# Kernel tuning notes

Hardware: AMD Instinct MI355X
Metric: run time of the kernel (lower is better)

The kernel has to match this reference:

```python
import jax, jax.numpy as jnp
import numpy as np

D_IN = 1024
D_OUT = 1024
NUM_HEADS = 16
HEAD_DIM = D_OUT // NUM_HEADS


def setup_inputs() -> dict:
    key = jax.random.key(0)
    ks = jax.random.split(key, 6)
    scale = 0.02
    x = jax.random.normal(ks[0], (2, 2048, D_IN), dtype=jnp.float32)
    Wq = jax.random.normal(ks[1], (D_IN, D_OUT), dtype=jnp.float32) * scale
    Wk = jax.random.normal(ks[2], (D_IN, D_OUT), dtype=jnp.float32) * scale
    Wv = jax.random.normal(ks[3], (D_IN, D_OUT), dtype=jnp.float32) * scale
    Wo = jax.random.normal(ks[4], (D_OUT, D_OUT), dtype=jnp.float32) * scale
    bo = jax.random.normal(ks[5], (D_OUT,), dtype=jnp.float32) * scale
    return {"x": x, "Wq": Wq, "Wk": Wk, "Wv": Wv, "Wo": Wo, "bo": bo}


def reference(x, Wq, Wk, Wv, Wo, bo):
    b, T, _ = x.shape
    h, dh = NUM_HEADS, HEAD_DIM
    # QKV projections (no bias), split heads: [b,T,d_out] -> [b,h,T,dh]
    q = (x @ Wq).reshape(b, T, h, dh).transpose(0, 2, 1, 3)
    k = (x @ Wk).reshape(b, T, h, dh).transpose(0, 2, 1, 3)
    v = (x @ Wv).reshape(b, T, h, dh).transpose(0, 2, 1, 3)
    # scaled dot-product scores with causal mask
    scores = jnp.einsum("bhqd,bhkd->bhqk", q, k) / jnp.sqrt(jnp.float32(dh))
    causal = jnp.tril(jnp.ones((T, T), dtype=bool))  # True = allowed
    scores = jnp.where(causal, scores, -jnp.inf)
    attn = jax.nn.softmax(scores, axis=-1)
    # dropout p=0.0 -> identity
    ctx = jnp.einsum("bhqk,bhkd->bhqd", attn, v)
    ctx = ctx.transpose(0, 2, 1, 3).reshape(b, T, h * dh)
    return ctx @ Wo + bo
```

## Files before the change

kernel.cpp:

```cpp
#include <hip/hip_runtime.h>

typedef __attribute__((ext_vector_type(8))) __bf16 bf16x8;
typedef __attribute__((ext_vector_type(4))) __bf16 bf16x4;
typedef __attribute__((ext_vector_type(4))) float  f32x4;

static constexpr int TSEQ    = 2048;
static constexpr int DMODEL  = 1024;
static constexpr int HD      = 64;
static constexpr int VSTRIDE = 2080;
static constexpr int LSTR    = 72;

#define AS1 __attribute__((address_space(1)))
#define AS3 __attribute__((address_space(3)))

__global__ __launch_bounds__(256) void k_prep(const float* __restrict__ x,
    const float* __restrict__ w0, const float* __restrict__ w1,
    const float* __restrict__ w2, const float* __restrict__ w3,
    __bf16* __restrict__ xbf, __bf16* __restrict__ wt_all) {
  __shared__ float tile[32][33];
  const int blk = blockIdx.x;
  const int tid = threadIdx.x;
  if (blk < 4096) {
    size_t i = ((size_t)blk * 256 + tid) * 4;
    float4 v = *(const float4*)(x + i);
    bf16x4 o = { (__bf16)v.x, (__bf16)v.y, (__bf16)v.z, (__bf16)v.w };
    *(bf16x4*)(xbf + i) = o;
    return;
  }
  const int tz = blk - 4096;
  const int wi = tz >> 10;
  const int tl = tz & 1023;
  const int n0 = (tl & 31) * 32, k0 = (tl >> 5) * 32;
  const float* w = wi == 0 ? w0 : wi == 1 ? w1 : wi == 2 ? w2 : w3;
  __bf16* out = wt_all + (size_t)wi * DMODEL * DMODEL;
  const int tx = tid & 31, ty0 = (tid >> 5) * 4;
#pragma unroll
  for (int j = 0; j < 4; j++)
    tile[ty0 + j][tx] = w[(size_t)(k0 + ty0 + j) * DMODEL + n0 + tx];
  __syncthreads();
#pragma unroll
  for (int j = 0; j < 4; j++)
    out[(size_t)(n0 + ty0 + j) * DMODEL + k0 + tx] = (__bf16)tile[tx][ty0 + j];
}

template <int NB>
__device__ __forceinline__ void gemm_mainloop_p(const __bf16* __restrict__ A,
                                                const __bf16* __restrict__ Bt,
                                                int bm, int bn,
                                                __bf16* At, __bf16* Bl,
                                                f32x4 acc[4][NB / 32]) {
  constexpr int NT = NB / 32;
  const int tid  = threadIdx.x;
  const int lane = tid & 63;
  const int l15  = lane & 15, quad = lane >> 4;
  const int wv   = tid >> 6;
  const int wm   = (wv >> 1) * 64, wn = (wv & 1) * (NT * 16);
  const int srow = lane >> 2;
  const int scol = (lane & 3) << 3;

  auto stage = [&](int k0, int hb) {
#pragma unroll
    for (int ss = 0; ss < 2; ss++) {
      const int s   = wv * 2 + ss;
      const int row = s * 16 + srow;
      __builtin_amdgcn_global_load_lds(
          (const AS1 void*)(A + (size_t)(bm + row) * 1024 + k0 + scol),
          (AS3 void*)(At + hb * 4096 + s * 512), 16, 0, 0);
    }
#pragma unroll
    for (int ss = 0; ss < NB / 64; ss++) {
      const int s   = wv * (NB / 64) + ss;
      const int row = s * 16 + srow;
      __builtin_amdgcn_global_load_lds(
          (const AS1 void*)(Bt + (size_t)(bn + row) * 1024 + k0 + scol),
          (AS3 void*)(Bl + hb * (NB * 32) + s * 512), 16, 0, 0);
    }
  };

  stage(0, 0);
  for (int k0 = 0; k0 < 1024; k0 += 32) {
    const int cur = (k0 >> 5) & 1;
    __syncthreads();
    bf16x8 af[4], bfr[NT];
#pragma unroll
    for (int mt = 0; mt < 4; mt++)
      af[mt] = *(const bf16x8*)(At + cur * 4096 + (wm + mt * 16 + l15) * 32 + quad * 8);
#pragma unroll
    for (int nt = 0; nt < NT; nt++)
      bfr[nt] = *(const bf16x8*)(Bl + cur * (NB * 32) + (wn + nt * 16 + l15) * 32 + quad * 8);
    if (k0 + 32 < 1024) stage(k0 + 32, cur ^ 1);
#pragma unroll
    for (int mt = 0; mt < 4; mt++)
#pragma unroll
      for (int nt = 0; nt < NT; nt++)
        acc[mt][nt] = __builtin_amdgcn_mfma_f32_16x16x32_bf16(
            af[mt], bfr[nt], acc[mt][nt], 0, 0, 0);
  }
}

__global__ __launch_bounds__(256) void k_gemm_qkv(const __bf16* __restrict__ xbf,
    const __bf16* __restrict__ wt_all, __bf16* __restrict__ qws,
    __bf16* __restrict__ kws, __bf16* __restrict__ vtws) {
  __shared__ __bf16 At[2 * 128 * 32];
  __shared__ __bf16 Bl[2 * 128 * 32];
  const int which = blockIdx.z;
  const __bf16* wt = wt_all + (size_t)which * DMODEL * DMODEL;
  const int bm = blockIdx.y * 128, bn = blockIdx.x * 128;
  f32x4 acc[4][4];
  const f32x4 z = {0.f, 0.f, 0.f, 0.f};
#pragma unroll
  for (int mt = 0; mt < 4; mt++)
#pragma unroll
    for (int nt = 0; nt < 4; nt++) acc[mt][nt] = z;
  gemm_mainloop_p<128>(xbf, wt, bm, bn, At, Bl, acc);
  const int lane = threadIdx.x & 63;
  const int l15 = lane & 15, quad = lane >> 4;
  const int wv = threadIdx.x >> 6;
  const int wm = (wv >> 1) * 64, wn = (wv & 1) * 64;
#pragma unroll
  for (int mt = 0; mt < 4; mt++)
#pragma unroll
    for (int nt = 0; nt < 4; nt++)
#pragma unroll
      for (int r = 0; r < 4; r++) {
        int m = bm + wm + mt * 16 + quad * 4 + r;
        int n = bn + wn + nt * 16 + l15;
        int b = m >> 11, t = m & 2047;
        int h = n >> 6,  d = n & 63;
        int bh = b * 16 + h;
        float av = acc[mt][nt][r];
        if (which == 0)      qws[((size_t)bh * TSEQ + t) * HD + d] = (__bf16)(av * 0.18033688f);
        else if (which == 1) kws[((size_t)bh * TSEQ + t) * HD + d] = (__bf16)av;
        else                 vtws[((size_t)bh * HD + d) * VSTRIDE + t] = (__bf16)av;
      }
}

__global__ __launch_bounds__(256) void k_attn(const __bf16* __restrict__ qws,
    const __bf16* __restrict__ kws, const __bf16* __restrict__ vtws,
    __bf16* __restrict__ ctx) {
  const int bh  = blockIdx.x & 31;
  const int qb0 = blockIdx.x >> 5, qb1 = 31 - qb0;
  const int tid = threadIdx.x;
  const int lane = tid & 63, wv = tid >> 6;
  const int l15 = lane & 15, quad = lane >> 4;
  const __bf16* qp = qws  + (size_t)bh * TSEQ * HD;
  const __bf16* kp = kws  + (size_t)bh * TSEQ * HD;
  const __bf16* vp = vtws + (size_t)bh * HD * VSTRIDE;
  const int b = bh >> 4, h = bh & 15;

  __shared__ __bf16 kbuf[2][64 * LSTR];
  __shared__ __bf16 vbuf[2][64 * LSTR];
  __shared__ __bf16 plds[4][16 * LSTR];

  const f32x4 z = {0.f, 0.f, 0.f, 0.f};
  const int sr = tid >> 3, sc = (tid & 7) * 8;

  const int qr0a = qb0 * 64 + wv * 16;
  const int qr0b = qb1 * 64 + wv * 16;
  bf16x8 aq0[2], aq1[2];
#pragma unroll
  for (int kb = 0; kb < 2; kb++) {
    aq0[kb] = *(const bf16x8*)(qp + (size_t)(qr0a + l15) * HD + kb * 32 + quad * 8);
    aq1[kb] = *(const bf16x8*)(qp + (size_t)(qr0b + l15) * HD + kb * 32 + quad * 8);
  }

  bf16x8 kreg[2], vreg[2];
  kreg[0] = *(const bf16x8*)(kp + (size_t)sr * HD + sc);
  kreg[1] = *(const bf16x8*)(kp + (size_t)(sr + 32) * HD + sc);
  vreg[0] = *(const bf16x8*)(vp + (size_t)sr * VSTRIDE + sc);
  vreg[1] = *(const bf16x8*)(vp + (size_t)(sr + 32) * VSTRIDE + sc);
  *(bf16x8*)(kbuf[0] + sr * LSTR + sc)        = kreg[0];
  *(bf16x8*)(kbuf[0] + (sr + 32) * LSTR + sc) = kreg[1];
  *(bf16x8*)(vbuf[0] + sr * LSTR + sc)        = vreg[0];
  *(bf16x8*)(vbuf[0] + (sr + 32) * LSTR + sc) = vreg[1];
  __syncthreads();

  float lpart[4] = {0.f, 0.f, 0.f, 0.f};
  f32x4 acc[4];
#pragma unroll
  for (int dt = 0; dt < 4; dt++) acc[dt] = z;

  for (int s = 0; s < 33; s++) {
    const int cur = s & 1;
    const bool h0 = (s <= qb0);
    const bool masked = (s == qb0) || (s == 32);

    if (s + 1 < 33) {
      const int ktn = (s + 1 <= qb0) ? (s + 1) * 64 : (s - qb0) * 64;
      kreg[0] = *(const bf16x8*)(kp + (size_t)(ktn + sr) * HD + sc);
      kreg[1] = *(const bf16x8*)(kp + (size_t)(ktn + sr + 32) * HD + sc);
      vreg[0] = *(const bf16x8*)(vp + (size_t)sr * VSTRIDE + ktn + sc);
      vreg[1] = *(const bf16x8*)(vp + (size_t)(sr + 32) * VSTRIDE + ktn + sc);
    }

    const __bf16* kb_ = kbuf[cur];
    const __bf16* vb_ = vbuf[cur];
    f32x4 sarr[4];
#pragma unroll
    for (int nt = 0; nt < 4; nt++) sarr[nt] = z;
#pragma unroll
    for (int nt = 0; nt < 4; nt++)
#pragma unroll
      for (int kb = 0; kb < 2; kb++) {
        bf16x8 bk = *(const bf16x8*)(kb_ + (nt * 16 + l15) * LSTR + kb * 32 + quad * 8);
        bf16x8 a  = h0 ? aq0[kb] : aq1[kb];
        sarr[nt] = __builtin_amdgcn_mfma_f32_16x16x32_bf16(a, bk, sarr[nt], 0, 0, 0);
      }
    if (masked) {
#pragma unroll
      for (int r = 0; r < 4; r++) {
        const int qloc = wv * 16 + quad * 4 + r;
#pragma unroll
        for (int nt = 0; nt < 4; nt++) {
          int kloc = nt * 16 + l15;
          float p = (kloc <= qloc) ? __builtin_amdgcn_exp2f(sarr[nt][r]) : 0.f;
          lpart[r] += p;
          plds[wv][(quad * 4 + r) * LSTR + nt * 16 + l15] = (__bf16)p;
        }
      }
    } else {
#pragma unroll
      for (int r = 0; r < 4; r++)
#pragma unroll
        for (int nt = 0; nt < 4; nt++) {
          float p = __builtin_amdgcn_exp2f(sarr[nt][r]);
          lpart[r] += p;
          plds[wv][(quad * 4 + r) * LSTR + nt * 16 + l15] = (__bf16)p;
        }
    }
#pragma unroll
    for (int kb = 0; kb < 2; kb++) {
      bf16x8 ap = *(const bf16x8*)(&plds[wv][l15 * LSTR + kb * 32 + quad * 8]);
#pragma unroll
      for (int dt = 0; dt < 4; dt++) {
        bf16x8 bvv = *(const bf16x8*)(vb_ + (dt * 16 + l15) * LSTR + kb * 32 + quad * 8);
        acc[dt] = __builtin_amdgcn_mfma_f32_16x16x32_bf16(ap, bvv, acc[dt], 0, 0, 0);
      }
    }

    if (s + 1 < 33) {
      const int nxt = cur ^ 1;
      *(bf16x8*)(kbuf[nxt] + sr * LSTR + sc)        = kreg[0];
      *(bf16x8*)(kbuf[nxt] + (sr + 32) * LSTR + sc) = kreg[1];
      *(bf16x8*)(vbuf[nxt] + sr * LSTR + sc)        = vreg[0];
      *(bf16x8*)(vbuf[nxt] + (sr + 32) * LSTR + sc) = vreg[1];
    }
    __syncthreads();

    if (masked) {
      const int qr0 = h0 ? qr0a : qr0b;
#pragma unroll
      for (int r = 0; r < 4; r++) {
        float l = lpart[r];
        l += __shfl_xor(l, 1, 64);
        l += __shfl_xor(l, 2, 64);
        l += __shfl_xor(l, 4, 64);
        l += __shfl_xor(l, 8, 64);
        float linv = 1.f / l;
        const int qrow = qr0 + quad * 4 + r;
#pragma unroll
        for (int dt = 0; dt < 4; dt++)
          ctx[((size_t)(b * TSEQ + qrow)) * DMODEL + h * 64 + dt * 16 + l15] =
              (__bf16)(acc[dt][r] * linv);
        lpart[r] = 0.f;
      }
#pragma unroll
      for (int dt = 0; dt < 4; dt++) acc[dt] = z;
    }
  }
}

__global__ __launch_bounds__(256) void k_gemm_out(const __bf16* __restrict__ ctx,
    const __bf16* __restrict__ wot, const float* __restrict__ bo,
    float* __restrict__ out) {
  __shared__ __bf16 At[2 * 128 * 32];
  __shared__ __bf16 Bl[2 * 64 * 32];
  const int bm = blockIdx.y * 128, bn = blockIdx.x * 64;
  f32x4 acc[4][2];
  const f32x4 z = {0.f, 0.f, 0.f, 0.f};
#pragma unroll
  for (int mt = 0; mt < 4; mt++)
#pragma unroll
    for (int nt = 0; nt < 2; nt++) acc[mt][nt] = z;
  gemm_mainloop_p<64>(ctx, wot, bm, bn, At, Bl, acc);
  const int lane = threadIdx.x & 63;
  const int l15 = lane & 15, quad = lane >> 4;
  const int wv = threadIdx.x >> 6;
  const int wm = (wv >> 1) * 64, wn = (wv & 1) * 32;
#pragma unroll
  for (int mt = 0; mt < 4; mt++)
#pragma unroll
    for (int nt = 0; nt < 2; nt++)
#pragma unroll
      for (int r = 0; r < 4; r++) {
        int m = bm + wm + mt * 16 + quad * 4 + r;
        int n = bn + wn + nt * 16 + l15;
        out[(size_t)m * DMODEL + n] = acc[mt][nt][r] + bo[n];
      }
}

extern "C" void kernel_launch(void* const* d_in, const int* in_sizes, int n_in,
                              void* d_out, int out_size, void* d_ws, size_t ws_size,
                              hipStream_t stream) {
  const float* x  = (const float*)d_in[0];
  const float* Wq = (const float*)d_in[1];
  const float* Wk = (const float*)d_in[2];
  const float* Wv = (const float*)d_in[3];
  const float* Wo = (const float*)d_in[4];
  const float* bo = (const float*)d_in[5];
  float* out = (float*)d_out;

  __bf16* xbf  = (__bf16*)d_ws;
  __bf16* wt   = xbf  + (size_t)4096 * 1024;
  __bf16* qws  = wt   + (size_t)4 * 1024 * 1024;
  __bf16* kws  = qws  + (size_t)32 * 2048 * 64;
  __bf16* vtws = kws  + (size_t)32 * 2048 * 64;
  __bf16* ctx  = xbf;

  k_prep<<<8192, 256, 0, stream>>>(x, Wq, Wk, Wv, Wo, xbf, wt);
  k_gemm_qkv<<<dim3(8, 32, 3), 256, 0, stream>>>(xbf, wt, qws, kws, vtws);
  k_attn<<<512, 256, 0, stream>>>(qws, kws, vtws, ctx);
  k_gemm_out<<<dim3(16, 32), 256, 0, stream>>>(ctx, wt + (size_t)3 * 1024 * 1024, bo, out);
}
```

Before: 184.3 us.

## Use BK=64 GEMM tiles with XOR-swizzled LDS and vectorized V-transpose stores

The shared GEMM mainloop now stages 64-wide K slices instead of 32, halving the number of barrier iterations. LDS rows are XOR-swizzled on the 16-byte column chunk to avoid bank conflicts on fragment reads. The next-stage prefetch is issued before the fragment loads. The QKV epilogue for V writes four consecutive timesteps as one bf16x4 store instead of scalar strided stores. LDS use per block doubles, which may lower occupancy.

New measurement: 194.5 us. 1.06x slower.

```diff
diff --git a/kernel.cpp b/kernel.cpp
--- a/kernel.cpp
+++ b/kernel.cpp
@@ -44,65 +44,78 @@
 }
 
 template <int NB>
-__device__ __forceinline__ void gemm_mainloop_p(const __bf16* __restrict__ A,
-                                                const __bf16* __restrict__ Bt,
-                                                int bm, int bn,
-                                                __bf16* At, __bf16* Bl,
-                                                f32x4 acc[4][NB / 32]) {
+__device__ __forceinline__ void gemm_mainloop2(const __bf16* __restrict__ A,
+                                               const __bf16* __restrict__ Bt,
+                                               int bm, int bn,
+                                               __bf16* At, __bf16* Bl,
+                                               f32x4 acc[4][NB / 32]) {
   constexpr int NT = NB / 32;
   const int tid  = threadIdx.x;
   const int lane = tid & 63;
   const int l15  = lane & 15, quad = lane >> 4;
   const int wv   = tid >> 6;
   const int wm   = (wv >> 1) * 64, wn = (wv & 1) * (NT * 16);
-  const int srow = lane >> 2;
-  const int scol = (lane & 3) << 3;
-
-  auto stage = [&](int k0, int hb) {
-#pragma unroll
-    for (int ss = 0; ss < 2; ss++) {
-      const int s   = wv * 2 + ss;
-      const int row = s * 16 + srow;
+  const int srl  = lane >> 3;
+  const int c8   = lane & 7;
+
+  auto stageA = [&](int k0, int hb) {
+#pragma unroll
+    for (int j = 0; j < 4; j++) {
+      const int row = wv * 32 + j * 8 + srl;
+      const int sc  = c8 ^ (row & 7);
       __builtin_amdgcn_global_load_lds(
-          (const AS1 void*)(A + (size_t)(bm + row) * 1024 + k0 + scol),
-          (AS3 void*)(At + hb * 4096 + s * 512), 16, 0, 0);
-    }
-#pragma unroll
-    for (int ss = 0; ss < NB / 64; ss++) {
-      const int s   = wv * (NB / 64) + ss;
-      const int row = s * 16 + srow;
+          (const AS1 void*)(A + (size_t)(bm + row) * 1024 + k0 + sc * 8),
+          (AS3 void*)(At + hb * 8192 + (wv * 32 + j * 8) * 64), 16, 0, 0);
+    }
+  };
+  auto stageB = [&](int k0, int hb) {
+#pragma unroll
+    for (int j = 0; j < NB / 32; j++) {
+      const int row = wv * (NB / 4) + j * 8 + srl;
+      const int sc  = c8 ^ (row & 7);
       __builtin_amdgcn_global_load_lds(
-          (const AS1 void*)(Bt + (size_t)(bn + row) * 1024 + k0 + scol),
-          (AS3 void*)(Bl + hb * (NB * 32) + s * 512), 16, 0, 0);
+          (const AS1 void*)(Bt + (size_t)(bn + row) * 1024 + k0 + sc * 8),
+          (AS3 void*)(Bl + hb * (NB * 64) + (wv * (NB / 4) + j * 8) * 64), 16, 0, 0);
     }
   };
 
-  stage(0, 0);
-  for (int k0 = 0; k0 < 1024; k0 += 32) {
-    const int cur = (k0 >> 5) & 1;
+  stageA(0, 0); stageB(0, 0);
+  for (int k0 = 0; k0 < 1024; k0 += 64) {
+    const int cur = (k0 >> 6) & 1;
     __syncthreads();
-    bf16x8 af[4], bfr[NT];
-#pragma unroll
-    for (int mt = 0; mt < 4; mt++)
-      af[mt] = *(const bf16x8*)(At + cur * 4096 + (wm + mt * 16 + l15) * 32 + quad * 8);
-#pragma unroll
-    for (int nt = 0; nt < NT; nt++)
-      bfr[nt] = *(const bf16x8*)(Bl + cur * (NB * 32) + (wn + nt * 16 + l15) * 32 + quad * 8);
-    if (k0 + 32 < 1024) stage(k0 + 32, cur ^ 1);
-#pragma unroll
-    for (int mt = 0; mt < 4; mt++)
-#pragma unroll
-      for (int nt = 0; nt < NT; nt++)
-        acc[mt][nt] = __builtin_amdgcn_mfma_f32_16x16x32_bf16(
-            af[mt], bfr[nt], acc[mt][nt], 0, 0, 0);
+    if (k0 + 64 < 1024) { stageA(k0 + 64, cur ^ 1); stageB(k0 + 64, cur ^ 1); }
+    bf16x8 af[2][4], bfr[2][NT];
+#pragma unroll
+    for (int ks = 0; ks < 2; ks++) {
+#pragma unroll
+      for (int mt = 0; mt < 4; mt++) {
+        const int row = wm + mt * 16 + l15;
+        af[ks][mt] = *(const bf16x8*)(At + cur * 8192 + row * 64 +
+                                      (((ks * 4 + quad) ^ (row & 7)) << 3));
+      }
+#pragma unroll
+      for (int nt = 0; nt < NT; nt++) {
+        const int row = wn + nt * 16 + l15;
+        bfr[ks][nt] = *(const bf16x8*)(Bl + cur * (NB * 64) + row * 64 +
+                                       (((ks * 4 + quad) ^ (row & 7)) << 3));
+      }
+    }
+#pragma unroll
+    for (int ks = 0; ks < 2; ks++)
+#pragma unroll
+      for (int mt = 0; mt < 4; mt++)
+#pragma unroll
+        for (int nt = 0; nt < NT; nt++)
+          acc[mt][nt] = __builtin_amdgcn_mfma_f32_16x16x32_bf16(
+              af[ks][mt], bfr[ks][nt], acc[mt][nt], 0, 0, 0);
   }
 }
 
 __global__ __launch_bounds__(256) void k_gemm_qkv(const __bf16* __restrict__ xbf,
     const __bf16* __restrict__ wt_all, __bf16* __restrict__ qws,
     __bf16* __restrict__ kws, __bf16* __restrict__ vtws) {
-  __shared__ __bf16 At[2 * 128 * 32];
-  __shared__ __bf16 Bl[2 * 128 * 32];
+  __shared__ __bf16 At[2 * 128 * 64];
+  __shared__ __bf16 Bl[2 * 128 * 64];
   const int which = blockIdx.z;
   const __bf16* wt = wt_all + (size_t)which * DMODEL * DMODEL;
   const int bm = blockIdx.y * 128, bn = blockIdx.x * 128;
@@ -112,27 +125,42 @@
   for (int mt = 0; mt < 4; mt++)
 #pragma unroll
     for (int nt = 0; nt < 4; nt++) acc[mt][nt] = z;
-  gemm_mainloop_p<128>(xbf, wt, bm, bn, At, Bl, acc);
+  gemm_mainloop2<128>(xbf, wt, bm, bn, At, Bl, acc);
   const int lane = threadIdx.x & 63;
   const int l15 = lane & 15, quad = lane >> 4;
   const int wv = threadIdx.x >> 6;
   const int wm = (wv >> 1) * 64, wn = (wv & 1) * 64;
-#pragma unroll
-  for (int mt = 0; mt < 4; mt++)
-#pragma unroll
-    for (int nt = 0; nt < 4; nt++)
-#pragma unroll
-      for (int r = 0; r < 4; r++) {
-        int m = bm + wm + mt * 16 + quad * 4 + r;
+  if (which == 2) {
+#pragma unroll
+    for (int mt = 0; mt < 4; mt++)
+#pragma unroll
+      for (int nt = 0; nt < 4; nt++) {
+        int t0 = bm + wm + mt * 16 + quad * 4;
         int n = bn + wn + nt * 16 + l15;
-        int b = m >> 11, t = m & 2047;
-        int h = n >> 6,  d = n & 63;
+        int h = n >> 6, d = n & 63;
+        int b = t0 >> 11;
         int bh = b * 16 + h;
-        float av = acc[mt][nt][r];
-        if (which == 0)      qws[((size_t)bh * TSEQ + t) * HD + d] = (__bf16)(av * 0.18033688f);
-        else if (which == 1) kws[((size_t)bh * TSEQ + t) * HD + d] = (__bf16)av;
-        else                 vtws[((size_t)bh * HD + d) * VSTRIDE + t] = (__bf16)av;
-      }
+        bf16x4 o = { (__bf16)acc[mt][nt][0], (__bf16)acc[mt][nt][1],
+                     (__bf16)acc[mt][nt][2], (__bf16)acc[mt][nt][3] };
+        *(bf16x4*)(vtws + ((size_t)bh * HD + d) * VSTRIDE + (t0 & 2047)) = o;
+      }
+  } else {
+#pragma unroll
+    for (int mt = 0; mt < 4; mt++)
+#pragma unroll
+      for (int nt = 0; nt < 4; nt++)
+#pragma unroll
+        for (int r = 0; r < 4; r++) {
+          int m = bm + wm + mt * 16 + quad * 4 + r;
+          int n = bn + wn + nt * 16 + l15;
+          int b = m >> 11, t = m & 2047;
+          int h = n >> 6,  d = n & 63;
+          int bh = b * 16 + h;
+          float av = acc[mt][nt][r];
+          if (which == 0) qws[((size_t)bh * TSEQ + t) * HD + d] = (__bf16)(av * 0.18033688f);
+          else            kws[((size_t)bh * TSEQ + t) * HD + d] = (__bf16)av;
+        }
+  }
 }
 
 __global__ __launch_bounds__(256) void k_attn(const __bf16* __restrict__ qws,
@@ -273,8 +301,8 @@
 __global__ __launch_bounds__(256) void k_gemm_out(const __bf16* __restrict__ ctx,
     const __bf16* __restrict__ wot, const float* __restrict__ bo,
     float* __restrict__ out) {
-  __shared__ __bf16 At[2 * 128 * 32];
-  __shared__ __bf16 Bl[2 * 64 * 32];
+  __shared__ __bf16 At[2 * 128 * 64];
+  __shared__ __bf16 Bl[2 * 64 * 64];
   const int bm = blockIdx.y * 128, bn = blockIdx.x * 64;
   f32x4 acc[4][2];
   const f32x4 z = {0.f, 0.f, 0.f, 0.f};
@@ -282,7 +310,7 @@
   for (int mt = 0; mt < 4; mt++)
 #pragma unroll
     for (int nt = 0; nt < 2; nt++) acc[mt][nt] = z;
-  gemm_mainloop_p<64>(ctx, wot, bm, bn, At, Bl, acc);
+  gemm_mainloop2<64>(ctx, wot, bm, bn, At, Bl, acc);
   const int lane = threadIdx.x & 63;
   const int l15 = lane & 15, quad = lane >> 4;
   const int wv = threadIdx.x >> 6;
```
